# Performance work log

Hardware: AMD Instinct MI355X
Metric: run time of the kernel (lower is better)

## Reference

```python
import jax, jax.numpy as jnp
import numpy as np

N = 100000
E = 1600000
NFEAT, NHID, NCLASS = 128, 128, 64


def setup_inputs() -> dict:
    key = jax.random.key(0)
    ks = jax.random.split(key, 8)
    x = jax.random.normal(ks[0], (N, NFEAT), dtype=jnp.float32)
    edge_index = jax.random.randint(ks[1], (2, E), 0, N, dtype=jnp.int32)
    def glorot(k, fan_in, fan_out):
        s = (6.0 / (fan_in + fan_out)) ** 0.5
        return jax.random.uniform(k, (fan_in, fan_out), jnp.float32, -s, s)
    W0 = glorot(ks[2], NFEAT, NHID)
    b0 = jnp.zeros((NHID,), jnp.float32)
    W1 = glorot(ks[3], NHID, NHID)
    b1 = jnp.zeros((NHID,), jnp.float32)
    W2 = glorot(ks[4], NHID, NCLASS)
    b2 = jnp.zeros((NCLASS,), jnp.float32)
    return {"x": x, "edge_index": edge_index, "W0": W0, "b0": b0,
            "W1": W1, "b1": b1, "W2": W2, "b2": b2}


def _normalized_adj(edge_index):
    # add self-loops (SparseTensor.set_diag)
    loops = jnp.arange(N, dtype=edge_index.dtype)
    row = jnp.concatenate([edge_index[0], loops])
    col = jnp.concatenate([edge_index[1], loops])
    ones = jnp.ones(row.shape[0], jnp.float32)
    deg = jax.ops.segment_sum(ones, row, num_segments=N)  # row sums incl. self-loop
    dis = jnp.where(deg > 0, deg ** -0.5, 0.0)
    w = dis[row] * dis[col]  # DAD: D^-1/2 A D^-1/2
    return row, col, w


def _spmm(row, col, w, h):
    # A @ h via gather + segment-sum: [E+N, d] intermediate
    return jax.ops.segment_sum(w[:, None] * h[col], row, num_segments=N)


def reference(x, edge_index, W0, b0, W1, b1, W2, b2):
    row, col, w = _normalized_adj(edge_index)
    h = x
    for Wl, bl, last in ((W0, b0, False), (W1, b1, False), (W2, b2, True)):
        h = _spmm(row, col, w, h @ Wl) + bl  # GCNConv(normalize=False)
        if not last:
            h = jax.nn.relu(h)  # dropout p=0.0 -> identity
    return h
```

## Files before the change

### kernel.cpp

```cpp
#include <hip/hip_runtime.h>



__device__ inline unsigned short f2bf(float f) {
    union { float f; unsigned u; } v; v.f = f;
    unsigned r = v.u + 0x7fffu + ((v.u >> 16) & 1u);
    return (unsigned short)(r >> 16);
}

__device__ inline void bf2x_to_f(unsigned u, float& a, float& b) {
    union { unsigned x; float f; } lo, hi;
    lo.x = u << 16; hi.x = u & 0xffff0000u;
    a = lo.f; b = hi.f;
}

__device__ inline void accum8(float* acc, uint4 u, float w) {
    float a, b;
    bf2x_to_f(u.x, a, b); acc[0] = fmaf(w, a, acc[0]); acc[1] = fmaf(w, b, acc[1]);
    bf2x_to_f(u.y, a, b); acc[2] = fmaf(w, a, acc[2]); acc[3] = fmaf(w, b, acc[3]);
    bf2x_to_f(u.z, a, b); acc[4] = fmaf(w, a, acc[4]); acc[5] = fmaf(w, b, acc[5]);
    bf2x_to_f(u.w, a, b); acc[6] = fmaf(w, a, acc[6]); acc[7] = fmaf(w, b, acc[7]);
}


__global__ void k_count(const int* __restrict__ row, int* __restrict__ deg,
                        int* __restrict__ pos, int e) {
    int i = blockIdx.x * blockDim.x + threadIdx.x;
    if (i < e) pos[i] = atomicAdd(&deg[row[i]], 1);
}

__global__ void k_dis(const int* __restrict__ deg, float* __restrict__ dis, int n) {
    int i = blockIdx.x * blockDim.x + threadIdx.x;
    if (i < n) dis[i] = rsqrtf((float)(deg[i] + 1));
}

__global__ void k_scan1(const int* __restrict__ deg, int* __restrict__ rp,
                        int* __restrict__ bsum, int n) {
    __shared__ int s[256];
    int tid = threadIdx.x;
    int i = blockIdx.x * 256 + tid;
    int v = (i < n) ? deg[i] : 0;
    s[tid] = v;
    __syncthreads();
    for (int off = 1; off < 256; off <<= 1) {
        int t = (tid >= off) ? s[tid - off] : 0;
        __syncthreads();
        s[tid] += t;
        __syncthreads();
    }
    if (i < n) rp[i] = s[tid] - v;
    if (tid == 255) bsum[blockIdx.x] = s[255];
}

__global__ void k_scan2(const int* __restrict__ bsum, int* __restrict__ boffs,
                        int nb, int* __restrict__ rp, int n, int total) {
    __shared__ int s[512];
    int tid = threadIdx.x;
    int v = (tid < nb) ? bsum[tid] : 0;
    s[tid] = v;
    __syncthreads();
    for (int off = 1; off < 512; off <<= 1) {
        int t = (tid >= off) ? s[tid - off] : 0;
        __syncthreads();
        s[tid] += t;
        __syncthreads();
    }
    if (tid < nb) boffs[tid] = s[tid] - v;
    if (tid == 0) rp[n] = total;
}

__global__ void k_scan3(int* __restrict__ rp, const int* __restrict__ boffs, int n) {
    int i = blockIdx.x * blockDim.x + threadIdx.x;
    if (i < n) rp[i] += boffs[i >> 8];
}

__global__ void k_scatter(const int* __restrict__ row, const int* __restrict__ col,
                          const int* __restrict__ rp, const int* __restrict__ pos,
                          int* __restrict__ csr, int e) {
    int i = blockIdx.x * blockDim.x + threadIdx.x;
    if (i < e) {
        int r = row[i];
        csr[rp[r] + pos[i]] = col[i];
    }
}


__global__ __launch_bounds__(256) void k_gemm(const float* __restrict__ H,
                                              const float* __restrict__ W,
                                              unsigned short* __restrict__ T,
                                              int n, int ldw) {
    __shared__ float Hs[64 * 128];
    __shared__ float Ws[128 * 64];
    const int tid = threadIdx.x;
    const int row0 = blockIdx.x * 64;
    const int col0 = blockIdx.y * 64;

#pragma unroll
    for (int i = 0; i < 8; i++) {
        int flat = i * 256 + tid;
        int r = flat >> 4, c4 = (flat & 15) * 4;
        *(float4*)&Ws[r * 64 + c4] = *(const float4*)&W[r * ldw + col0 + c4];
    }
#pragma unroll
    for (int i = 0; i < 8; i++) {
        int flat = i * 256 + tid;
        int r = flat >> 5, c4 = (flat & 31) * 4;
        int gr = row0 + r;
        float4 v = make_float4(0.f, 0.f, 0.f, 0.f);
        if (gr < n) v = *(const float4*)&H[(size_t)gr * 128 + c4];
        *(float4*)&Hs[r * 128 + c4] = v;
    }
    __syncthreads();

    const int tx = tid & 15, ty = tid >> 4;
    const int c0 = tx * 4;
    float4 acc[4];
#pragma unroll
    for (int j = 0; j < 4; j++) acc[j] = make_float4(0.f, 0.f, 0.f, 0.f);

    for (int k = 0; k < 128; k += 4) {
        float4 w0 = *(float4*)&Ws[(k + 0) * 64 + c0];
        float4 w1 = *(float4*)&Ws[(k + 1) * 64 + c0];
        float4 w2 = *(float4*)&Ws[(k + 2) * 64 + c0];
        float4 w3 = *(float4*)&Ws[(k + 3) * 64 + c0];
#pragma unroll
        for (int j = 0; j < 4; j++) {
            float4 h = *(float4*)&Hs[(ty + 16 * j) * 128 + k];
            acc[j].x = fmaf(h.x, w0.x, acc[j].x);
            acc[j].y = fmaf(h.x, w0.y, acc[j].y);
            acc[j].z = fmaf(h.x, w0.z, acc[j].z);
            acc[j].w = fmaf(h.x, w0.w, acc[j].w);
            acc[j].x = fmaf(h.y, w1.x, acc[j].x);
            acc[j].y = fmaf(h.y, w1.y, acc[j].y);
            acc[j].z = fmaf(h.y, w1.z, acc[j].z);
            acc[j].w = fmaf(h.y, w1.w, acc[j].w);
            acc[j].x = fmaf(h.z, w2.x, acc[j].x);
            acc[j].y = fmaf(h.z, w2.y, acc[j].y);
            acc[j].z = fmaf(h.z, w2.z, acc[j].z);
            acc[j].w = fmaf(h.z, w2.w, acc[j].w);
            acc[j].x = fmaf(h.w, w3.x, acc[j].x);
            acc[j].y = fmaf(h.w, w3.y, acc[j].y);
            acc[j].z = fmaf(h.w, w3.z, acc[j].z);
            acc[j].w = fmaf(h.w, w3.w, acc[j].w);
        }
    }
#pragma unroll
    for (int j = 0; j < 4; j++) {
        int gr = row0 + ty + 16 * j;
        if (gr < n) {
            ushort4 o;
            o.x = f2bf(acc[j].x); o.y = f2bf(acc[j].y);
            o.z = f2bf(acc[j].z); o.w = f2bf(acc[j].w);
            *(ushort4*)&T[(size_t)gr * ldw + col0 + c0] = o;
        }
    }
}


template <bool RELU>
__global__ void k_agg128(const unsigned short* __restrict__ T, float* __restrict__ O,
                         const int* __restrict__ rp, const int* __restrict__ cols,
                         const float* __restrict__ dis, const float* __restrict__ bias,
                         int n) {
    int wid = (blockIdx.x * blockDim.x + threadIdx.x) >> 6;
    int lane = threadIdx.x & 63;
    if (wid >= n) return;
    const int quad = lane >> 4;
    const int fl = (lane & 15) * 8;
    int beg = rp[wid], end = rp[wid + 1];
    float di = dis[wid];

    float acc[8] = {0.f, 0.f, 0.f, 0.f, 0.f, 0.f, 0.f, 0.f};
    int e = beg + quad;
    for (; e + 4 < end; e += 8) {
        int c0 = cols[e];
        int c1 = cols[e + 4];
        float w0 = dis[c0];
        float w1 = dis[c1];
        uint4 u0 = *(const uint4*)&T[(size_t)c0 * 128 + fl];
        uint4 u1 = *(const uint4*)&T[(size_t)c1 * 128 + fl];
        accum8(acc, u0, w0);
        accum8(acc, u1, w1);
    }
    if (e < end) {
        int c0 = cols[e];
        float w0 = dis[c0];
        uint4 u0 = *(const uint4*)&T[(size_t)c0 * 128 + fl];
        accum8(acc, u0, w0);
    }
#pragma unroll
    for (int k = 0; k < 8; k++) {
        acc[k] += __shfl_xor(acc[k], 16);
        acc[k] += __shfl_xor(acc[k], 32);
    }
    if (quad == 0) {
        uint4 us = *(const uint4*)&T[(size_t)wid * 128 + fl];
        float self[8];
        bf2x_to_f(us.x, self[0], self[1]);
        bf2x_to_f(us.y, self[2], self[3]);
        bf2x_to_f(us.z, self[4], self[5]);
        bf2x_to_f(us.w, self[6], self[7]);
        float4 bA = *(const float4*)&bias[fl];
        float4 bB = *(const float4*)&bias[fl + 4];
        float bb[8] = {bA.x, bA.y, bA.z, bA.w, bB.x, bB.y, bB.z, bB.w};
        float dii = di * di;
        float o[8];
#pragma unroll
        for (int k = 0; k < 8; k++) {
            o[k] = fmaf(di, acc[k], fmaf(dii, self[k], bb[k]));
            if (RELU) o[k] = fmaxf(o[k], 0.f);
        }
        *(float4*)&O[(size_t)wid * 128 + fl] = make_float4(o[0], o[1], o[2], o[3]);
        *(float4*)&O[(size_t)wid * 128 + fl + 4] = make_float4(o[4], o[5], o[6], o[7]);
    }
}

template <bool RELU>
__global__ void k_agg64(const unsigned short* __restrict__ T, float* __restrict__ O,
                        const int* __restrict__ rp, const int* __restrict__ cols,
                        const float* __restrict__ dis, const float* __restrict__ bias,
                        int n) {
    int wid = (blockIdx.x * blockDim.x + threadIdx.x) >> 6;
    int lane = threadIdx.x & 63;
    if (wid >= n) return;
    const int oct = lane >> 3;
    const int fl = (lane & 7) * 8;
    int beg = rp[wid], end = rp[wid + 1];
    float di = dis[wid];

    float acc[8] = {0.f, 0.f, 0.f, 0.f, 0.f, 0.f, 0.f, 0.f};
    int e = beg + oct;
    for (; e + 8 < end; e += 16) {
        int c0 = cols[e];
        int c1 = cols[e + 8];
        float w0 = dis[c0];
        float w1 = dis[c1];
        uint4 u0 = *(const uint4*)&T[(size_t)c0 * 64 + fl];
        uint4 u1 = *(const uint4*)&T[(size_t)c1 * 64 + fl];
        accum8(acc, u0, w0);
        accum8(acc, u1, w1);
    }
    if (e < end) {
        int c0 = cols[e];
        float w0 = dis[c0];
        uint4 u0 = *(const uint4*)&T[(size_t)c0 * 64 + fl];
        accum8(acc, u0, w0);
    }
#pragma unroll
    for (int k = 0; k < 8; k++) {
        acc[k] += __shfl_xor(acc[k], 8);
        acc[k] += __shfl_xor(acc[k], 16);
        acc[k] += __shfl_xor(acc[k], 32);
    }
    if (oct == 0) {
        uint4 us = *(const uint4*)&T[(size_t)wid * 64 + fl];
        float self[8];
        bf2x_to_f(us.x, self[0], self[1]);
        bf2x_to_f(us.y, self[2], self[3]);
        bf2x_to_f(us.z, self[4], self[5]);
        bf2x_to_f(us.w, self[6], self[7]);
        float4 bA = *(const float4*)&bias[fl];
        float4 bB = *(const float4*)&bias[fl + 4];
        float bb[8] = {bA.x, bA.y, bA.z, bA.w, bB.x, bB.y, bB.z, bB.w};
        float dii = di * di;
        float o[8];
#pragma unroll
        for (int k = 0; k < 8; k++) {
            o[k] = fmaf(di, acc[k], fmaf(dii, self[k], bb[k]));
            if (RELU) o[k] = fmaxf(o[k], 0.f);
        }
        *(float4*)&O[(size_t)wid * 64 + fl] = make_float4(o[0], o[1], o[2], o[3]);
        *(float4*)&O[(size_t)wid * 64 + fl + 4] = make_float4(o[4], o[5], o[6], o[7]);
    }
}


static inline char* align256(char* p) {
    return (char*)(((uintptr_t)p + 255) & ~(uintptr_t)255);
}

extern "C" void kernel_launch(void* const* d_in, const int* in_sizes, int n_in,
                              void* d_out, int out_size, void* d_ws, size_t ws_size,
                              hipStream_t stream) {
    const float* x  = (const float*)d_in[0];
    const int*   ei = (const int*)d_in[1];
    const float* W0 = (const float*)d_in[2];
    const float* b0 = (const float*)d_in[3];
    const float* W1 = (const float*)d_in[4];
    const float* b1 = (const float*)d_in[5];
    const float* W2 = (const float*)d_in[6];
    const float* b2 = (const float*)d_in[7];

    const int Nn = in_sizes[0] / 128;
    const int Ee = in_sizes[1] / 2;
    const int* rowI = ei;
    const int* colI = ei + Ee;

    char* p = (char*)d_ws;
    float* bufF = (float*)p;            p += (size_t)Nn * 128 * 4; p = align256(p);
    unsigned short* Tb = (unsigned short*)p; p += (size_t)Nn * 128 * 2; p = align256(p);
    int* csr    = (int*)p;   p += (size_t)Ee * 4;       p = align256(p);
    int* pos    = (int*)p;   p += (size_t)Ee * 4;       p = align256(p);
    int* rp     = (int*)p;   p += (size_t)(Nn + 1) * 4; p = align256(p);
    int* deg    = (int*)p;   p += (size_t)Nn * 4;       p = align256(p);
    float* dis  = (float*)p; p += (size_t)Nn * 4;       p = align256(p);
    int* bsum   = (int*)p;   p += 512 * 4;
    int* boffs  = (int*)p;   p += 512 * 4;

    const int eb = (Ee + 255) / 256;
    const int nb = (Nn + 255) / 256;

    hipMemsetAsync(deg, 0, (size_t)Nn * 4, stream);

    k_count<<<eb, 256, 0, stream>>>(rowI, deg, pos, Ee);
    k_dis<<<nb, 256, 0, stream>>>(deg, dis, Nn);
    k_scan1<<<nb, 256, 0, stream>>>(deg, rp, bsum, Nn);
    k_scan2<<<1, 512, 0, stream>>>(bsum, boffs, nb, rp, Nn, Ee);
    k_scan3<<<nb, 256, 0, stream>>>(rp, boffs, Nn);
    k_scatter<<<eb, 256, 0, stream>>>(rowI, colI, rp, pos, csr, Ee);

    dim3 g2((Nn + 63) / 64, 2);
    dim3 g1((Nn + 63) / 64, 1);
    const int ab = (Nn + 3) / 4;

    k_gemm<<<g2, 256, 0, stream>>>(x, W0, Tb, Nn, 128);
    k_agg128<true><<<ab, 256, 0, stream>>>(Tb, bufF, rp, csr, dis, b0, Nn);
    k_gemm<<<g2, 256, 0, stream>>>(bufF, W1, Tb, Nn, 128);
    k_agg128<true><<<ab, 256, 0, stream>>>(Tb, bufF, rp, csr, dis, b1, Nn);
    k_gemm<<<g1, 256, 0, stream>>>(bufF, W2, Tb, Nn, 64);
    k_agg64<false><<<ab, 256, 0, stream>>>(Tb, (float*)d_out, rp, csr, dis, b2, Nn);
}
```

Measured before the change: 515.9 us.

## Replace FP32 SIMT GEMMs with split-bf16 MFMA GEMMs and bf16 hi/lo activations

The scalar FP32 dense transforms become MFMA 16x16x32 bf16 GEMMs. Near-FP32 accuracy is kept by splitting each operand into bf16 high and low parts and issuing three MFMAs per tile. The aggregation kernels now write activations directly as hi/lo bf16 pairs, and new prep kernels split the input features and transpose the weights up front. This targets the ALU-bound SIMT GEMM cost, at the price of extra prep launches and 3x MFMA work.

```diff
diff --git a/kernel.cpp b/kernel.cpp
--- a/kernel.cpp
+++ b/kernel.cpp
@@ -1,11 +1,24 @@
 #include <hip/hip_runtime.h>
 
+
+typedef __attribute__((ext_vector_type(8))) short bf16x8;
+typedef __attribute__((ext_vector_type(4))) float floatx4;
 
 
 __device__ inline unsigned short f2bf(float f) {
     union { float f; unsigned u; } v; v.f = f;
     unsigned r = v.u + 0x7fffu + ((v.u >> 16) & 1u);
     return (unsigned short)(r >> 16);
+}
+
+__device__ inline float bf2f(unsigned short h) {
+    union { unsigned u; float f; } v; v.u = (unsigned)h << 16;
+    return v.f;
+}
+
+__device__ inline void split_bf(float v, unsigned short& h, unsigned short& l) {
+    h = f2bf(v);
+    l = f2bf(v - bf2f(h));
 }
 
 __device__ inline void bf2x_to_f(unsigned u, float& a, float& b) {
@@ -85,80 +98,125 @@
 }
 
 
-__global__ __launch_bounds__(256) void k_gemm(const float* __restrict__ H,
-                                              const float* __restrict__ W,
-                                              unsigned short* __restrict__ T,
-                                              int n, int ldw) {
-    __shared__ float Hs[64 * 128];
-    __shared__ float Ws[128 * 64];
+__global__ void k_prepX(const float* __restrict__ X, unsigned short* __restrict__ Xhi,
+                        unsigned short* __restrict__ Xlo, int total4) {
+    int id = blockIdx.x * blockDim.x + threadIdx.x;
+    if (id < total4) {
+        float4 v = ((const float4*)X)[id];
+        ushort4 h, l;
+        split_bf(v.x, h.x, l.x);
+        split_bf(v.y, h.y, l.y);
+        split_bf(v.z, h.z, l.z);
+        split_bf(v.w, h.w, l.w);
+        ((ushort4*)Xhi)[id] = h;
+        ((ushort4*)Xlo)[id] = l;
+    }
+}
+
+__global__ void k_prepW(const float* __restrict__ W, unsigned short* __restrict__ Wthi,
+                        unsigned short* __restrict__ Wtlo, int ldw) {
+    int id = blockIdx.x * blockDim.x + threadIdx.x;
+    if (id < 128 * ldw) {
+        int k = id / ldw, nn = id - k * ldw;
+        unsigned short h, l;
+        split_bf(W[id], h, l);
+        Wthi[nn * 128 + k] = h;
+        Wtlo[nn * 128 + k] = l;
+    }
+}
+
+
+template <int NB>
+__global__ __launch_bounds__(256) void k_gemm_mfma(
+    const unsigned short* __restrict__ Ahi, const unsigned short* __restrict__ Alo,
+    const unsigned short* __restrict__ Wthi, const unsigned short* __restrict__ Wtlo,
+    unsigned short* __restrict__ T, int n) {
+    const int LDW = NB * 64;
+    __shared__ unsigned short Ah_s[64 * 128];
+    __shared__ unsigned short Al_s[64 * 128];
     const int tid = threadIdx.x;
-    const int row0 = blockIdx.x * 64;
-    const int col0 = blockIdx.y * 64;
-
-#pragma unroll
-    for (int i = 0; i < 8; i++) {
-        int flat = i * 256 + tid;
-        int r = flat >> 4, c4 = (flat & 15) * 4;
-        *(float4*)&Ws[r * 64 + c4] = *(const float4*)&W[r * ldw + col0 + c4];
-    }
-#pragma unroll
-    for (int i = 0; i < 8; i++) {
-        int flat = i * 256 + tid;
-        int r = flat >> 5, c4 = (flat & 31) * 4;
+    const int bid = blockIdx.x;
+    const int bx = (NB == 2) ? (bid >> 1) : bid;
+    const int by = (NB == 2) ? (bid & 1) : 0;
+    const int row0 = bx * 64;
+    const int col0 = by * 64;
+
+    const int wave = tid >> 6, lane = tid & 63;
+    const int ln = lane & 15, quad = lane >> 4;
+    const int m0 = (wave >> 1) * 32;
+    const int nq0 = (wave & 1) * 32;
+
+    bf16x8 Bh[4][2], Bl[4][2];
+#pragma unroll
+    for (int s = 0; s < 4; s++)
+#pragma unroll
+        for (int j = 0; j < 2; j++) {
+            int ncol = col0 + nq0 + 16 * j + ln;
+            int koff = 32 * s + quad * 8;
+            Bh[s][j] = *(const bf16x8*)&Wthi[ncol * 128 + koff];
+            Bl[s][j] = *(const bf16x8*)&Wtlo[ncol * 128 + koff];
+        }
+
+#pragma unroll
+    for (int k = 0; k < 4; k++) {
+        int id = k * 256 + tid;
+        int r = id >> 4, c = id & 15;
         int gr = row0 + r;
-        float4 v = make_float4(0.f, 0.f, 0.f, 0.f);
-        if (gr < n) v = *(const float4*)&H[(size_t)gr * 128 + c4];
-        *(float4*)&Hs[r * 128 + c4] = v;
+        uint4 vh = make_uint4(0, 0, 0, 0), vl = make_uint4(0, 0, 0, 0);
+        if (gr < n) {
+            vh = *(const uint4*)&Ahi[(size_t)gr * 128 + c * 8];
+            vl = *(const uint4*)&Alo[(size_t)gr * 128 + c * 8];
+        }
+        int pc = c ^ (r & 15);
+        *(uint4*)&Ah_s[r * 128 + pc * 8] = vh;
+        *(uint4*)&Al_s[r * 128 + pc * 8] = vl;
     }
     __syncthreads();
 
-    const int tx = tid & 15, ty = tid >> 4;
-    const int c0 = tx * 4;
-    float4 acc[4];
-#pragma unroll
-    for (int j = 0; j < 4; j++) acc[j] = make_float4(0.f, 0.f, 0.f, 0.f);
-
-    for (int k = 0; k < 128; k += 4) {
-        float4 w0 = *(float4*)&Ws[(k + 0) * 64 + c0];
-        float4 w1 = *(float4*)&Ws[(k + 1) * 64 + c0];
-        float4 w2 = *(float4*)&Ws[(k + 2) * 64 + c0];
-        float4 w3 = *(float4*)&Ws[(k + 3) * 64 + c0];
-#pragma unroll
-        for (int j = 0; j < 4; j++) {
-            float4 h = *(float4*)&Hs[(ty + 16 * j) * 128 + k];
-            acc[j].x = fmaf(h.x, w0.x, acc[j].x);
-            acc[j].y = fmaf(h.x, w0.y, acc[j].y);
-            acc[j].z = fmaf(h.x, w0.z, acc[j].z);
-            acc[j].w = fmaf(h.x, w0.w, acc[j].w);
-            acc[j].x = fmaf(h.y, w1.x, acc[j].x);
-            acc[j].y = fmaf(h.y, w1.y, acc[j].y);
-            acc[j].z = fmaf(h.y, w1.z, acc[j].z);
-            acc[j].w = fmaf(h.y, w1.w, acc[j].w);
-            acc[j].x = fmaf(h.z, w2.x, acc[j].x);
-            acc[j].y = fmaf(h.z, w2.y, acc[j].y);
-            acc[j].z = fmaf(h.z, w2.z, acc[j].z);
-            acc[j].w = fmaf(h.z, w2.w, acc[j].w);
-            acc[j].x = fmaf(h.w, w3.x, acc[j].x);
-            acc[j].y = fmaf(h.w, w3.y, acc[j].y);
-            acc[j].z = fmaf(h.w, w3.z, acc[j].z);
-            acc[j].w = fmaf(h.w, w3.w, acc[j].w);
+    floatx4 acc[2][2];
+#pragma unroll
+    for (int i = 0; i < 2; i++)
+#pragma unroll
+        for (int j = 0; j < 2; j++) acc[i][j] = (floatx4){0.f, 0.f, 0.f, 0.f};
+
+#pragma unroll
+    for (int s = 0; s < 4; s++) {
+        bf16x8 ah[2], al[2];
+#pragma unroll
+        for (int i = 0; i < 2; i++) {
+            int off = (m0 + 16 * i + ln) * 128 + ((4 * s + quad) ^ ln) * 8;
+            ah[i] = *(const bf16x8*)&Ah_s[off];
+            al[i] = *(const bf16x8*)&Al_s[off];
         }
-    }
-#pragma unroll
-    for (int j = 0; j < 4; j++) {
-        int gr = row0 + ty + 16 * j;
-        if (gr < n) {
-            ushort4 o;
-            o.x = f2bf(acc[j].x); o.y = f2bf(acc[j].y);
-            o.z = f2bf(acc[j].z); o.w = f2bf(acc[j].w);
-            *(ushort4*)&T[(size_t)gr * ldw + col0 + c0] = o;
-        }
-    }
-}
-
-
-template <bool RELU>
-__global__ void k_agg128(const unsigned short* __restrict__ T, float* __restrict__ O,
+#pragma unroll
+        for (int i = 0; i < 2; i++)
+#pragma unroll
+            for (int j = 0; j < 2; j++) {
+                acc[i][j] = __builtin_amdgcn_mfma_f32_16x16x32_bf16(
+                    ah[i], Bh[s][j], acc[i][j], 0, 0, 0);
+                acc[i][j] = __builtin_amdgcn_mfma_f32_16x16x32_bf16(
+                    ah[i], Bl[s][j], acc[i][j], 0, 0, 0);
+                acc[i][j] = __builtin_amdgcn_mfma_f32_16x16x32_bf16(
+                    al[i], Bh[s][j], acc[i][j], 0, 0, 0);
+            }
+    }
+
+#pragma unroll
+    for (int i = 0; i < 2; i++)
+#pragma unroll
+        for (int j = 0; j < 2; j++)
+#pragma unroll
+            for (int reg = 0; reg < 4; reg++) {
+                int gr = row0 + m0 + 16 * i + quad * 4 + reg;
+                int gc = col0 + nq0 + 16 * j + ln;
+                if (gr < n) T[(size_t)gr * LDW + gc] = f2bf(acc[i][j][reg]);
+            }
+}
+
+
+__global__ void k_agg128(const unsigned short* __restrict__ T,
+                         unsigned short* __restrict__ Ohi,
+                         unsigned short* __restrict__ Olo,
                          const int* __restrict__ rp, const int* __restrict__ cols,
                          const float* __restrict__ dis, const float* __restrict__ bias,
                          int n) {
@@ -204,18 +262,22 @@
         float4 bB = *(const float4*)&bias[fl + 4];
         float bb[8] = {bA.x, bA.y, bA.z, bA.w, bB.x, bB.y, bB.z, bB.w};
         float dii = di * di;
-        float o[8];
+        unsigned short h[8], l[8];
 #pragma unroll
         for (int k = 0; k < 8; k++) {
-            o[k] = fmaf(di, acc[k], fmaf(dii, self[k], bb[k]));
-            if (RELU) o[k] = fmaxf(o[k], 0.f);
+            float o = fmaf(di, acc[k], fmaf(dii, self[k], bb[k]));
+            o = fmaxf(o, 0.f);
+            split_bf(o, h[k], l[k]);
         }
-        *(float4*)&O[(size_t)wid * 128 + fl] = make_float4(o[0], o[1], o[2], o[3]);
-        *(float4*)&O[(size_t)wid * 128 + fl + 4] = make_float4(o[4], o[5], o[6], o[7]);
-    }
-}
-
-template <bool RELU>
+        ushort4 h0 = {h[0], h[1], h[2], h[3]}, h1 = {h[4], h[5], h[6], h[7]};
+        ushort4 l0 = {l[0], l[1], l[2], l[3]}, l1 = {l[4], l[5], l[6], l[7]};
+        *(ushort4*)&Ohi[(size_t)wid * 128 + fl] = h0;
+        *(ushort4*)&Ohi[(size_t)wid * 128 + fl + 4] = h1;
+        *(ushort4*)&Olo[(size_t)wid * 128 + fl] = l0;
+        *(ushort4*)&Olo[(size_t)wid * 128 + fl + 4] = l1;
+    }
+}
+
 __global__ void k_agg64(const unsigned short* __restrict__ T, float* __restrict__ O,
                         const int* __restrict__ rp, const int* __restrict__ cols,
                         const float* __restrict__ dis, const float* __restrict__ bias,
@@ -265,10 +327,8 @@
         float dii = di * di;
         float o[8];
 #pragma unroll
-        for (int k = 0; k < 8; k++) {
+        for (int k = 0; k < 8; k++)
             o[k] = fmaf(di, acc[k], fmaf(dii, self[k], bb[k]));
-            if (RELU) o[k] = fmaxf(o[k], 0.f);
-        }
         *(float4*)&O[(size_t)wid * 64 + fl] = make_float4(o[0], o[1], o[2], o[3]);
         *(float4*)&O[(size_t)wid * 64 + fl + 4] = make_float4(o[4], o[5], o[6], o[7]);
     }
@@ -297,8 +357,9 @@
     const int* colI = ei + Ee;
 
     char* p = (char*)d_ws;
-    float* bufF = (float*)p;            p += (size_t)Nn * 128 * 4; p = align256(p);
-    unsigned short* Tb = (unsigned short*)p; p += (size_t)Nn * 128 * 2; p = align256(p);
+    unsigned short* Tb  = (unsigned short*)p; p += (size_t)Nn * 128 * 2; p = align256(p);
+    unsigned short* Ahi = (unsigned short*)p; p += (size_t)Nn * 128 * 2; p = align256(p);
+    unsigned short* Alo = (unsigned short*)p; p += (size_t)Nn * 128 * 2; p = align256(p);
     int* csr    = (int*)p;   p += (size_t)Ee * 4;       p = align256(p);
     int* pos    = (int*)p;   p += (size_t)Ee * 4;       p = align256(p);
     int* rp     = (int*)p;   p += (size_t)(Nn + 1) * 4; p = align256(p);
@@ -306,6 +367,12 @@
     float* dis  = (float*)p; p += (size_t)Nn * 4;       p = align256(p);
     int* bsum   = (int*)p;   p += 512 * 4;
     int* boffs  = (int*)p;   p += 512 * 4;
+    unsigned short* Wt0h = (unsigned short*)p; p += 128 * 128 * 2;
+    unsigned short* Wt0l = (unsigned short*)p; p += 128 * 128 * 2;
+    unsigned short* Wt1h = (unsigned short*)p; p += 128 * 128 * 2;
+    unsigned short* Wt1l = (unsigned short*)p; p += 128 * 128 * 2;
+    unsigned short* Wt2h = (unsigned short*)p; p += 64 * 128 * 2;
+    unsigned short* Wt2l = (unsigned short*)p; p += 64 * 128 * 2;
 
     const int eb = (Ee + 255) / 256;
     const int nb = (Nn + 255) / 256;
@@ -319,14 +386,18 @@
     k_scan3<<<nb, 256, 0, stream>>>(rp, boffs, Nn);
     k_scatter<<<eb, 256, 0, stream>>>(rowI, colI, rp, pos, csr, Ee);
 
-    dim3 g2((Nn + 63) / 64, 2);
-    dim3 g1((Nn + 63) / 64, 1);
+    k_prepX<<<(Nn * 32 + 255) / 256, 256, 0, stream>>>(x, Ahi, Alo, Nn * 32);
+    k_prepW<<<64, 256, 0, stream>>>(W0, Wt0h, Wt0l, 128);
+    k_prepW<<<64, 256, 0, stream>>>(W1, Wt1h, Wt1l, 128);
+    k_prepW<<<32, 256, 0, stream>>>(W2, Wt2h, Wt2l, 64);
+
+    const int gx = (Nn + 63) / 64;
     const int ab = (Nn + 3) / 4;
 
-    k_gemm<<<g2, 256, 0, stream>>>(x, W0, Tb, Nn, 128);
-    k_agg128<true><<<ab, 256, 0, stream>>>(Tb, bufF, rp, csr, dis, b0, Nn);
-    k_gemm<<<g2, 256, 0, stream>>>(bufF, W1, Tb, Nn, 128);
-    k_agg128<true><<<ab, 256, 0, stream>>>(Tb, bufF, rp, csr, dis, b1, Nn);
-    k_gemm<<<g1, 256, 0, stream>>>(bufF, W2, Tb, Nn, 64);
-    k_agg64<false><<<ab, 256, 0, stream>>>(Tb, (float*)d_out, rp, csr, dis, b2, Nn);
-}
+    k_gemm_mfma<2><<<2 * gx, 256, 0, stream>>>(Ahi, Alo, Wt0h, Wt0l, Tb, Nn);
+    k_agg128<<<ab, 256, 0, stream>>>(Tb, Ahi, Alo, rp, csr, dis, b0, Nn);
+    k_gemm_mfma<2><<<2 * gx, 256, 0, stream>>>(Ahi, Alo, Wt1h, Wt1l, Tb, Nn);
+    k_agg128<<<ab, 256, 0, stream>>>(Tb, Ahi, Alo, rp, csr, dis, b1, Nn);
+    k_gemm_mfma<1><<<gx, 256, 0, stream>>>(Ahi, Alo, Wt2h, Wt2l, Tb, Nn);
+    k_agg64<<<ab, 256, 0, stream>>>(Tb, (float*)d_out, rp, csr, dis, b2, Nn);
+}
```

Result: faster. 496.3 us (-3.8%).
